# Kernel optimization log

Hardware: AMD Instinct MI355X
Metric: run time of the kernel (lower is better)

The kernel has to match this reference:

```python
import jax, jax.numpy as jnp
import numpy as np

EPS_H = 1.0   # smooth Heaviside / delta regularization
MAX_ITER = 10


def _chan_vese_step(phi, I, dt, lam):
    # phi, I: [B, 512, H, W]
    px = jnp.gradient(phi, axis=3)
    py = jnp.gradient(phi, axis=2)
    nrm = jnp.sqrt(px * px + py * py + 1e-8)
    curv = jnp.gradient(px / nrm, axis=3) + jnp.gradient(py / nrm, axis=2)
    # smooth Heaviside and region means (per batch, per channel)
    H = 0.5 * (1.0 + (2.0 / jnp.pi) * jnp.arctan(phi / EPS_H))
    a1 = jnp.sum(H, axis=(2, 3), keepdims=True)
    a2 = jnp.sum(1.0 - H, axis=(2, 3), keepdims=True)
    c1 = jnp.sum(I * H, axis=(2, 3), keepdims=True) / (a1 + 1e-8)
    c2 = jnp.sum(I * (1.0 - H), axis=(2, 3), keepdims=True) / (a2 + 1e-8)
    delta = (EPS_H / jnp.pi) / (phi * phi + EPS_H * EPS_H)
    force = curv - lam * (I - c1) ** 2 + lam * (I - c2) ** 2
    return phi + dt * delta * force


def setup_inputs() -> dict:
    key = jax.random.key(0)
    ks = jax.random.split(key, 6)
    B, C, Hh, Ww = 8, 256, 64, 64
    contour = jax.random.normal(ks[0], (B, C, Hh, Ww), dtype=jnp.float32)
    g = jax.random.normal(ks[1], (B, C, Hh, Ww), dtype=jnp.float32)
    x = jax.random.normal(ks[2], (B, 2 * C, Hh, Ww), dtype=jnp.float32)
    dt = jnp.array([0.1], dtype=jnp.float32)
    lambda_ = jnp.array([1.0], dtype=jnp.float32)
    # 1x1 conv weights (no bias), stored as [out_ch, in_ch]
    g_w = jax.random.normal(ks[3], (512, C), dtype=jnp.float32) / np.sqrt(C)
    x_w = jax.random.normal(ks[4], (512, 2 * C), dtype=jnp.float32) / np.sqrt(2 * C)
    c_w = jax.random.normal(ks[5], (512, C), dtype=jnp.float32) / np.sqrt(C)
    return {"contour": contour, "g": g, "x": x, "dt": dt, "lambda_": lambda_,
            "g_w": g_w, "x_w": x_w, "c_w": c_w}


def reference(contour, g, x, dt, lambda_, g_w, x_w, c_w):
    # z = relu(g_conv(g)) + x_conv(x); 1x1 convs are per-pixel GEMMs
    z = jax.nn.relu(jnp.einsum('bchw,oc->bohw', g, g_w)) \
        + jnp.einsum('bchw,oc->bohw', x, x_w)
    phi0 = jnp.einsum('bchw,oc->bohw', contour, c_w)
    # bicubic resize of phi0 to z's spatial size is identity (same H, W)
    dts = dt[0]
    lam = lambda_[0]
    def step(phi, _):
        return _chan_vese_step(phi, z, dts, lam), None
    phi, _ = jax.lax.scan(step, phi0, None, length=MAX_ITER)
    return jax.nn.sigmoid(phi)
```

## Files before the change

kernel.cpp:

```cpp
#include <hip/hip_runtime.h>
#include <math.h>

#define PIX 4096
#define O_CH 512
#define CV_PITCH 80
#define CV_SSTR 20
#define NY_PITCH 36

#define WOFF_G 0
#define WOFF_X 131072
#define WOFF_C 393216
#define W_ELEMS 524288

typedef __attribute__((ext_vector_type(8))) short s16x8;
typedef __attribute__((ext_vector_type(4))) float f32x4;
typedef __attribute__((ext_vector_type(2))) float f32x2;

__device__ __forceinline__ unsigned cvt_pk_bf16(float a, float b) {
  unsigned r;
  asm("v_cvt_pk_bf16_f32 %0, %1, %2" : "=v"(r) : "v"(a), "v"(b));
  return r;
}

__global__ __launch_bounds__(256) void conv_w(
    const float* __restrict__ gw, const float* __restrict__ xw,
    const float* __restrict__ cw,
    ushort* __restrict__ WH, ushort* __restrict__ WL)
{
  const int r = blockIdx.y;
  const float* src = (r == 0) ? gw : ((r == 1) ? xw : cw);
  const int n4 = (r == 1) ? 65536 : 32768;
  const int doff = (r == 0) ? WOFF_G : ((r == 1) ? WOFF_X : WOFF_C);
  const int i = blockIdx.x * 256 + threadIdx.x;
  if (i >= n4) return;
  float4 v = ((const float4*)src)[i];
  unsigned h01 = cvt_pk_bf16(v.x, v.y);
  unsigned h23 = cvt_pk_bf16(v.z, v.w);
  float l0 = v.x - __uint_as_float(h01 << 16);
  float l1 = v.y - __uint_as_float(h01 & 0xffff0000u);
  float l2 = v.z - __uint_as_float(h23 << 16);
  float l3 = v.w - __uint_as_float(h23 & 0xffff0000u);
  unsigned lo01 = cvt_pk_bf16(l0, l1);
  unsigned lo23 = cvt_pk_bf16(l2, l3);
  ((uint2*)(WH + doff))[i] = make_uint2(h01, h23);
  ((uint2*)(WL + doff))[i] = make_uint2(lo01, lo23);
}

__global__ __launch_bounds__(256, 2) void mfma_gemm_all(
    const float* __restrict__ g, const float* __restrict__ x,
    const float* __restrict__ contour,
    const ushort* __restrict__ WHg, const ushort* __restrict__ WLg,
    float* __restrict__ z, float* __restrict__ phi0)
{
  __shared__ ushort WHs[8192], WLs[8192], AHs[8192], ALs[8192];
  const int t = threadIdx.x;
  const int lane = t & 63, wave = t >> 6;
  const int wm = wave >> 1, wn = wave & 1;
  const int rowA = lane & 15, kg = lane >> 4;
  const int pb = blockIdx.x * 128, ob = blockIdx.y * 128;
  const int bz = blockIdx.z;
  const bool isZ = bz < 8;
  const int b = isZ ? bz : bz - 8;

  const int woff1 = isZ ? WOFF_G : WOFF_C;
  const int K1 = 256;
  const float* A1 = (isZ ? g : contour) + (size_t)b * K1 * PIX;
  const int K2 = 512;
  const float* A2 = isZ ? x + (size_t)b * K2 * PIX : nullptr;
  float* out = (isZ ? z : phi0) + (size_t)b * O_CH * PIX;

  f32x4 acc[4][4];
#pragma unroll
  for (int mi = 0; mi < 4; ++mi)
#pragma unroll
    for (int ni = 0; ni < 4; ++ni) acc[mi][ni] = (f32x4){0.f, 0.f, 0.f, 0.f};

  for (int pass = 0; pass < 2; ++pass) {
    if (pass == 1 && A2 == nullptr) break;
    const int K = pass ? K2 : K1;
    const int woff = pass ? WOFF_X : woff1;
    const float* A = pass ? A2 : A1;

    for (int kb = 0; kb < K; kb += 64) {
      {
        const int o_r = t >> 1, hf = t & 1;
        const size_t wbase = (size_t)woff + (size_t)(ob + o_r) * K + kb + hf * 32;
        const ushort* whrow = WHg + wbase;
        const ushort* wlrow = WLg + wbase;
#pragma unroll
        for (int i = 0; i < 4; ++i) {
          int idx = o_r * 64 + (((hf * 4 + i) ^ (o_r & 7)) << 3);
          *(s16x8*)&WHs[idx] = *(const s16x8*)(whrow + i * 8);
          *(s16x8*)&WLs[idx] = *(const s16x8*)(wlrow + i * 8);
        }
      }
#pragma unroll
      for (int ph = 0; ph < 2; ++ph) {
        const int rp = ph * 64 + lane;
        const float* ac = A + (size_t)kb * PIX + pb + rp;
#pragma unroll
        for (int ch = 0; ch < 2; ++ch) {
          const int kloc0 = ch * 32 + wave * 8;
          float v[8];
#pragma unroll
          for (int j = 0; j < 8; ++j) v[j] = ac[(size_t)(kloc0 + j) * PIX];
          unsigned h[4], l[4];
#pragma unroll
          for (int j2 = 0; j2 < 4; ++j2) {
            h[j2] = cvt_pk_bf16(v[2 * j2], v[2 * j2 + 1]);
            float lo0 = v[2 * j2] - __uint_as_float(h[j2] << 16);
            float lo1 = v[2 * j2 + 1] - __uint_as_float(h[j2] & 0xffff0000u);
            l[j2] = cvt_pk_bf16(lo0, lo1);
          }
          int grp = ch * 4 + wave;
          int idx = rp * 64 + ((grp ^ (rp & 7)) << 3);
          *(uint4*)&AHs[idx] = make_uint4(h[0], h[1], h[2], h[3]);
          *(uint4*)&ALs[idx] = make_uint4(l[0], l[1], l[2], l[3]);
        }
      }
      __syncthreads();
#pragma unroll
      for (int ks = 0; ks < 2; ++ks) {
        s16x8 wh[4], wlv[4], ah[4], alv[4];
#pragma unroll
        for (int mi = 0; mi < 4; ++mi) {
          int row = wm * 64 + mi * 16 + rowA;
          int idx = row * 64 + (((ks * 4 + kg) ^ (row & 7)) << 3);
          wh[mi]  = *(const s16x8*)&WHs[idx];
          wlv[mi] = *(const s16x8*)&WLs[idx];
        }
#pragma unroll
        for (int ni = 0; ni < 4; ++ni) {
          int row = wn * 64 + ni * 16 + rowA;
          int idx = row * 64 + (((ks * 4 + kg) ^ (row & 7)) << 3);
          ah[ni]  = *(const s16x8*)&AHs[idx];
          alv[ni] = *(const s16x8*)&ALs[idx];
        }
#pragma unroll
        for (int mi = 0; mi < 4; ++mi)
#pragma unroll
          for (int ni = 0; ni < 4; ++ni) {
            acc[mi][ni] = __builtin_amdgcn_mfma_f32_16x16x32_bf16(wh[mi],  ah[ni],  acc[mi][ni], 0, 0, 0);
            acc[mi][ni] = __builtin_amdgcn_mfma_f32_16x16x32_bf16(wh[mi],  alv[ni], acc[mi][ni], 0, 0, 0);
            acc[mi][ni] = __builtin_amdgcn_mfma_f32_16x16x32_bf16(wlv[mi], ah[ni],  acc[mi][ni], 0, 0, 0);
          }
      }
      __syncthreads();
    }
    if (pass == 0 && isZ) {
#pragma unroll
      for (int mi = 0; mi < 4; ++mi)
#pragma unroll
        for (int ni = 0; ni < 4; ++ni)
#pragma unroll
          for (int r = 0; r < 4; ++r) acc[mi][ni][r] = fmaxf(acc[mi][ni][r], 0.f);
    }
  }
  const int orow = (lane >> 4) * 4, pcol = lane & 15;
#pragma unroll
  for (int mi = 0; mi < 4; ++mi)
#pragma unroll
    for (int ni = 0; ni < 4; ++ni)
#pragma unroll
      for (int r = 0; r < 4; ++r)
        out[(size_t)(ob + wm * 64 + mi * 16 + orow + r) * PIX +
            pb + wn * 64 + ni * 16 + pcol] = acc[mi][ni][r];
}

__device__ __forceinline__ float fast_atan(float x) {
  float a = __builtin_fabsf(x);
  float inv = __builtin_amdgcn_rcpf(a);
  bool big = a > 1.f;
  float tt = big ? inv : a;
  float t2 = tt * tt;
  float p = fmaf(t2, 0.0208351f, -0.0851330f);
  p = fmaf(t2, p, 0.1801410f);
  p = fmaf(t2, p, -0.3302995f);
  p = fmaf(t2, p, 0.9998660f);
  p = p * tt;
  float r = big ? (1.57079632679f - p) : p;
  return __builtin_copysignf(r, x);
}

__global__ __launch_bounds__(256, 4) void chanvese(
    const float* __restrict__ zb, float* __restrict__ ob,
    const float* __restrict__ dtp, const float* __restrict__ lamp)
{
  __shared__ float phi_l[64 * CV_PITCH];
  __shared__ unsigned ny_l[64 * NY_PITCH];
  __shared__ float red[12];
  const int t = threadIdx.x;
  const int lane = t & 63, wv = t >> 6;
  const int row = t >> 2, s = t & 3;
  const size_t gbase = (size_t)blockIdx.x * PIX + row * 64 + s * 16;
  const float dtv = dtp[0], lam = lamp[0];
  const float INV_PI = 0.31830988618379067f;
  const float dtpi = dtv * INV_PI;
  const float fy = (row == 0 || row == 63) ? 1.f : 0.5f;
  const float exl = (s == 0) ? 2.f : 1.f;
  const float exr = (s == 3) ? 2.f : 1.f;
  const int my  = row * CV_PITCH + s * CV_SSTR;
  const int ub  = ((row == 0) ? 0 : row - 1) * CV_PITCH + s * CV_SSTR;
  const int db  = ((row == 63) ? 63 : row + 1) * CV_PITCH + s * CV_SSTR;
  const int myn = row * NY_PITCH + s * 8;
  const int ubn = ((row == 0) ? 0 : row - 1) * NY_PITCH + s * 8;
  const int dbn = ((row == 63) ? 63 : row + 1) * NY_PITCH + s * 8;
  const f32x2 eps2 = {1e-8f, 1e-8f};

  f32x2 I2[8], ph2[8], nx2[8];
#pragma unroll
  for (int q = 0; q < 4; ++q) {
    f32x4 iv = *(const f32x4*)(zb + gbase + q * 4);
    f32x4 pv = *(const f32x4*)(ob + gbase + q * 4);
    I2[2 * q]     = (f32x2){iv[0], iv[1]};
    I2[2 * q + 1] = (f32x2){iv[2], iv[3]};
    ph2[2 * q]     = (f32x2){pv[0], pv[1]};
    ph2[2 * q + 1] = (f32x2){pv[2], pv[3]};
    *(f32x4*)&phi_l[my + q * 4] = pv;
  }
  float sI = 0.f, s_at = 0.f, s_iat = 0.f;
#pragma unroll
  for (int p = 0; p < 8; ++p) {
    sI += I2[p].x + I2[p].y;
    float a0 = fast_atan(ph2[p].x), a1 = fast_atan(ph2[p].y);
    s_at += a0 + a1;
    s_iat = fmaf(I2[p].x, a0, fmaf(I2[p].y, a1, s_iat));
  }
#pragma unroll
  for (int off = 32; off; off >>= 1) {
    sI += __shfl_xor(sI, off);
    s_at += __shfl_xor(s_at, off);
    s_iat += __shfl_xor(s_iat, off);
  }
  if (lane == 0) { red[wv] = s_at; red[4 + wv] = s_iat; red[8 + wv] = sI; }
  __syncthreads();
  float S_at = red[0] + red[1] + red[2] + red[3];
  float S_iat = red[4] + red[5] + red[6] + red[7];
  const float sumI = red[8] + red[9] + red[10] + red[11];

  for (int it = 0; it < 10; ++it) {
    float a1 = fmaf(INV_PI, S_at, 2048.f);
    float sIH = fmaf(INV_PI, S_iat, 0.5f * sumI);
    float c1 = sIH * __builtin_amdgcn_rcpf(a1 + 1e-8f);
    float c2 = (sumI - sIH) * __builtin_amdgcn_rcpf(4096.f - a1 + 1e-8f);
    float lam12 = lam * (c1 - c2);
    float ms12 = -(c1 + c2);

    float ls = __shfl(ph2[7].y, lane - 1);
    float rs = __shfl(ph2[0].x, lane + 1);
    float lb = (s == 0) ? ph2[0].x : ls;
    float rb = (s == 3) ? ph2[7].y : rs;
    unsigned nyp[8];
#pragma unroll
    for (int q = 0; q < 4; ++q) {
      f32x4 uv = *(const f32x4*)&phi_l[ub + q * 4];
      f32x4 dv = *(const f32x4*)&phi_l[db + q * 4];
#pragma unroll
      for (int e = 0; e < 2; ++e) {
        const int p = 2 * q + e;
        f32x2 u2 = (f32x2){uv[2 * e], uv[2 * e + 1]};
        f32x2 d2 = (f32x2){dv[2 * e], dv[2 * e + 1]};
        f32x2 py = (d2 - u2) * fy;
        f32x2 L = {(p == 0) ? lb : ph2[p - 1].y, ph2[p].x};
        f32x2 R = {ph2[p].y, (p == 7) ? rb : ph2[p + 1].x};
        f32x2 px = (R - L) * 0.5f;
        if (p == 0) px.x *= exl;
        if (p == 7) px.y *= exr;
        f32x2 qq = px * px + (py * py + eps2);
        f32x2 rn = {__builtin_amdgcn_rsqf(qq.x), __builtin_amdgcn_rsqf(qq.y)};
        nx2[p] = px * rn;
        f32x2 nyv = py * rn;
        nyp[p] = cvt_pk_bf16(nyv.x, nyv.y);
      }
    }
    *(uint4*)&ny_l[myn]     = make_uint4(nyp[0], nyp[1], nyp[2], nyp[3]);
    *(uint4*)&ny_l[myn + 4] = make_uint4(nyp[4], nyp[5], nyp[6], nyp[7]);
    __syncthreads();

    float nls = __shfl(nx2[7].y, lane - 1);
    float nrs = __shfl(nx2[0].x, lane + 1);
    float nlb = (s == 0) ? nx2[0].x : nls;
    float nrb = (s == 3) ? nx2[7].y : nrs;
    f32x2 inc_at2 = {0.f, 0.f}, inc_iat2 = {0.f, 0.f};
#pragma unroll
    for (int h = 0; h < 2; ++h) {
      uint4 au = *(const uint4*)&ny_l[ubn + 4 * h];
      uint4 ad = *(const uint4*)&ny_l[dbn + 4 * h];
      unsigned ua[4] = {au.x, au.y, au.z, au.w};
      unsigned ud[4] = {ad.x, ad.y, ad.z, ad.w};
      f32x2 phs[4];
#pragma unroll
      for (int e = 0; e < 4; ++e) {
        const int p = 4 * h + e;
        f32x2 nyu = {__uint_as_float(ua[e] << 16), __uint_as_float(ua[e] & 0xffff0000u)};
        f32x2 nyd = {__uint_as_float(ud[e] << 16), __uint_as_float(ud[e] & 0xffff0000u)};
        f32x2 dny = (nyd - nyu) * fy;
        f32x2 L = {(p == 0) ? nlb : nx2[p - 1].y, nx2[p].x};
        f32x2 R = {nx2[p].y, (p == 7) ? nrb : nx2[p + 1].x};
        f32x2 dnx = (R - L) * 0.5f;
        if (p == 0) dnx.x *= exl;
        if (p == 7) dnx.y *= exr;
        f32x2 curv = dnx + dny;
        f32x2 c = ph2[p];
        f32x2 den = c * c + (f32x2){1.f, 1.f};
        f32x2 rcd = {__builtin_amdgcn_rcpf(den.x), __builtin_amdgcn_rcpf(den.y)};
        f32x2 tI = I2[p] * 2.f + ms12;
        f32x2 force = tI * lam12 + curv;
        f32x2 dphi = (rcd * dtpi) * force;
        f32x2 pn = c + dphi;
        ph2[p] = pn;
        phs[e] = pn;
        f32x2 da = dphi * rcd;
        inc_at2 += da;
        inc_iat2 = I2[p] * da + inc_iat2;
      }
      if (it < 9) {
        *(f32x4*)&phi_l[my + 8 * h] =
            (f32x4){phs[0].x, phs[0].y, phs[1].x, phs[1].y};
        *(f32x4*)&phi_l[my + 8 * h + 4] =
            (f32x4){phs[2].x, phs[2].y, phs[3].x, phs[3].y};
      }
    }
    if (it < 9) {
      float inc_at = inc_at2.x + inc_at2.y;
      float inc_iat = inc_iat2.x + inc_iat2.y;
#pragma unroll
      for (int off = 32; off; off >>= 1) {
        inc_at += __shfl_xor(inc_at, off);
        inc_iat += __shfl_xor(inc_iat, off);
      }
      if (lane == 0) { red[2 * wv] = inc_at; red[2 * wv + 1] = inc_iat; }
      __syncthreads();
      S_at += red[0] + red[2] + red[4] + red[6];
      S_iat += red[1] + red[3] + red[5] + red[7];
    }
  }

#pragma unroll
  for (int q = 0; q < 4; ++q) {
    f32x2 pa = ph2[2 * q], pb2 = ph2[2 * q + 1];
    float o0 = 1.f / (1.f + exp2f(pa.x * -1.44269504089f));
    float o1 = 1.f / (1.f + exp2f(pa.y * -1.44269504089f));
    float o2 = 1.f / (1.f + exp2f(pb2.x * -1.44269504089f));
    float o3 = 1.f / (1.f + exp2f(pb2.y * -1.44269504089f));
    *(float4*)(ob + gbase + q * 4) = make_float4(o0, o1, o2, o3);
  }
}

extern "C" void kernel_launch(void* const* d_in, const int* in_sizes, int n_in,
                              void* d_out, int out_size, void* d_ws, size_t ws_size,
                              hipStream_t stream)
{
  const float* contour = (const float*)d_in[0];
  const float* g       = (const float*)d_in[1];
  const float* x       = (const float*)d_in[2];
  const float* dt      = (const float*)d_in[3];
  const float* lam     = (const float*)d_in[4];
  const float* g_w     = (const float*)d_in[5];
  const float* x_w     = (const float*)d_in[6];
  const float* c_w     = (const float*)d_in[7];
  float* out = (float*)d_out;
  float* z   = (float*)d_ws;
  ushort* WH = (ushort*)(z + (size_t)8 * O_CH * PIX);
  ushort* WL = WH + W_ELEMS;

  conv_w<<<dim3(256, 3), dim3(256), 0, stream>>>(g_w, x_w, c_w, WH, WL);
  mfma_gemm_all<<<dim3(32, 4, 16), dim3(256), 0, stream>>>(
      g, x, contour, WH, WL, z, out);
  chanvese<<<dim3(4096), dim3(256), 0, stream>>>(z, out, dt, lam);
}
```

Before: 246.0 us.

## Software-pipeline activation loads in GEMM with register prefetch of next K-step

Flattens the two-pass K loop into one step loop of 12 or 4 steps and prefetches the next step's fp32 activation tile into registers while the MFMAs run on the current shared-memory tile. The goal is to hide global load latency behind the matrix math. It raises register pressure under launch_bounds(256,2), which may cause spills or lower occupancy. It also makes a minor explicit vector broadcast change in the Chan-Vese step.

```diff
diff --git a/kernel.cpp b/kernel.cpp
--- a/kernel.cpp
+++ b/kernel.cpp
@@ -63,11 +63,10 @@
   const int b = isZ ? bz : bz - 8;
 
   const int woff1 = isZ ? WOFF_G : WOFF_C;
-  const int K1 = 256;
-  const float* A1 = (isZ ? g : contour) + (size_t)b * K1 * PIX;
-  const int K2 = 512;
-  const float* A2 = isZ ? x + (size_t)b * K2 * PIX : nullptr;
+  const float* A1 = (isZ ? g : contour) + (size_t)b * 256 * PIX;
+  const float* A2 = x + (size_t)(isZ ? b : 0) * 512 * PIX;
   float* out = (isZ ? z : phi0) + (size_t)b * O_CH * PIX;
+  const int nsteps = isZ ? 12 : 4;
 
   f32x4 acc[4][4];
 #pragma unroll
@@ -75,79 +74,104 @@
 #pragma unroll
     for (int ni = 0; ni < 4; ++ni) acc[mi][ni] = (f32x4){0.f, 0.f, 0.f, 0.f};
 
-  for (int pass = 0; pass < 2; ++pass) {
-    if (pass == 1 && A2 == nullptr) break;
-    const int K = pass ? K2 : K1;
-    const int woff = pass ? WOFF_X : woff1;
-    const float* A = pass ? A2 : A1;
-
-    for (int kb = 0; kb < K; kb += 64) {
-      {
-        const int o_r = t >> 1, hf = t & 1;
-        const size_t wbase = (size_t)woff + (size_t)(ob + o_r) * K + kb + hf * 32;
-        const ushort* whrow = WHg + wbase;
-        const ushort* wlrow = WLg + wbase;
-#pragma unroll
-        for (int i = 0; i < 4; ++i) {
-          int idx = o_r * 64 + (((hf * 4 + i) ^ (o_r & 7)) << 3);
-          *(s16x8*)&WHs[idx] = *(const s16x8*)(whrow + i * 8);
-          *(s16x8*)&WLs[idx] = *(const s16x8*)(wlrow + i * 8);
+  float pf[2][2][8];
+
+#pragma unroll
+  for (int ph = 0; ph < 2; ++ph) {
+    const float* acp = A1 + pb + ph * 64 + lane;
+#pragma unroll
+    for (int ch = 0; ch < 2; ++ch) {
+      const int kl0 = ch * 32 + wave * 8;
+#pragma unroll
+      for (int j = 0; j < 8; ++j)
+        pf[ph][ch][j] = acp[(size_t)(kl0 + j) * PIX];
+    }
+  }
+
+  for (int st = 0; st < nsteps; ++st) {
+    const bool s2 = st >= 4;
+    const int K = s2 ? 512 : 256;
+    const int woff = s2 ? WOFF_X : woff1;
+    const int kb = (s2 ? st - 4 : st) * 64;
+
+    {
+      const int o_r = t >> 1, hf = t & 1;
+      const size_t wbase = (size_t)woff + (size_t)(ob + o_r) * K + kb + hf * 32;
+      const ushort* whrow = WHg + wbase;
+      const ushort* wlrow = WLg + wbase;
+#pragma unroll
+      for (int i = 0; i < 4; ++i) {
+        int idx = o_r * 64 + (((hf * 4 + i) ^ (o_r & 7)) << 3);
+        *(s16x8*)&WHs[idx] = *(const s16x8*)(whrow + i * 8);
+        *(s16x8*)&WLs[idx] = *(const s16x8*)(wlrow + i * 8);
+      }
+    }
+#pragma unroll
+    for (int ph = 0; ph < 2; ++ph) {
+      const int rp = ph * 64 + lane;
+#pragma unroll
+      for (int ch = 0; ch < 2; ++ch) {
+        unsigned h[4], l[4];
+#pragma unroll
+        for (int j2 = 0; j2 < 4; ++j2) {
+          float v0 = pf[ph][ch][2 * j2], v1 = pf[ph][ch][2 * j2 + 1];
+          h[j2] = cvt_pk_bf16(v0, v1);
+          float lo0 = v0 - __uint_as_float(h[j2] << 16);
+          float lo1 = v1 - __uint_as_float(h[j2] & 0xffff0000u);
+          l[j2] = cvt_pk_bf16(lo0, lo1);
         }
-      }
+        int grp = ch * 4 + wave;
+        int idx = rp * 64 + ((grp ^ (rp & 7)) << 3);
+        *(uint4*)&AHs[idx] = make_uint4(h[0], h[1], h[2], h[3]);
+        *(uint4*)&ALs[idx] = make_uint4(l[0], l[1], l[2], l[3]);
+      }
+    }
+    __syncthreads();
+
+    if (st + 1 < nsteps) {
+      const bool n2 = (st + 1) >= 4;
+      const float* Ab = n2 ? A2 : A1;
+      const int kbn = (n2 ? st + 1 - 4 : st + 1) * 64;
 #pragma unroll
       for (int ph = 0; ph < 2; ++ph) {
-        const int rp = ph * 64 + lane;
-        const float* ac = A + (size_t)kb * PIX + pb + rp;
+        const float* acp = Ab + (size_t)kbn * PIX + pb + ph * 64 + lane;
 #pragma unroll
         for (int ch = 0; ch < 2; ++ch) {
-          const int kloc0 = ch * 32 + wave * 8;
-          float v[8];
-#pragma unroll
-          for (int j = 0; j < 8; ++j) v[j] = ac[(size_t)(kloc0 + j) * PIX];
-          unsigned h[4], l[4];
-#pragma unroll
-          for (int j2 = 0; j2 < 4; ++j2) {
-            h[j2] = cvt_pk_bf16(v[2 * j2], v[2 * j2 + 1]);
-            float lo0 = v[2 * j2] - __uint_as_float(h[j2] << 16);
-            float lo1 = v[2 * j2 + 1] - __uint_as_float(h[j2] & 0xffff0000u);
-            l[j2] = cvt_pk_bf16(lo0, lo1);
-          }
-          int grp = ch * 4 + wave;
-          int idx = rp * 64 + ((grp ^ (rp & 7)) << 3);
-          *(uint4*)&AHs[idx] = make_uint4(h[0], h[1], h[2], h[3]);
-          *(uint4*)&ALs[idx] = make_uint4(l[0], l[1], l[2], l[3]);
+          const int kl0 = ch * 32 + wave * 8;
+#pragma unroll
+          for (int j = 0; j < 8; ++j)
+            pf[ph][ch][j] = acp[(size_t)(kl0 + j) * PIX];
         }
       }
-      __syncthreads();
-#pragma unroll
-      for (int ks = 0; ks < 2; ++ks) {
-        s16x8 wh[4], wlv[4], ah[4], alv[4];
-#pragma unroll
-        for (int mi = 0; mi < 4; ++mi) {
-          int row = wm * 64 + mi * 16 + rowA;
-          int idx = row * 64 + (((ks * 4 + kg) ^ (row & 7)) << 3);
-          wh[mi]  = *(const s16x8*)&WHs[idx];
-          wlv[mi] = *(const s16x8*)&WLs[idx];
+    }
+
+#pragma unroll
+    for (int ks = 0; ks < 2; ++ks) {
+      s16x8 wh[4], wlv[4], ah[4], alv[4];
+#pragma unroll
+      for (int mi = 0; mi < 4; ++mi) {
+        int row = wm * 64 + mi * 16 + rowA;
+        int idx = row * 64 + (((ks * 4 + kg) ^ (row & 7)) << 3);
+        wh[mi]  = *(const s16x8*)&WHs[idx];
+        wlv[mi] = *(const s16x8*)&WLs[idx];
+      }
+#pragma unroll
+      for (int ni = 0; ni < 4; ++ni) {
+        int row = wn * 64 + ni * 16 + rowA;
+        int idx = row * 64 + (((ks * 4 + kg) ^ (row & 7)) << 3);
+        ah[ni]  = *(const s16x8*)&AHs[idx];
+        alv[ni] = *(const s16x8*)&ALs[idx];
+      }
+#pragma unroll
+      for (int mi = 0; mi < 4; ++mi)
+#pragma unroll
+        for (int ni = 0; ni < 4; ++ni) {
+          acc[mi][ni] = __builtin_amdgcn_mfma_f32_16x16x32_bf16(wh[mi],  ah[ni],  acc[mi][ni], 0, 0, 0);
+          acc[mi][ni] = __builtin_amdgcn_mfma_f32_16x16x32_bf16(wh[mi],  alv[ni], acc[mi][ni], 0, 0, 0);
+          acc[mi][ni] = __builtin_amdgcn_mfma_f32_16x16x32_bf16(wlv[mi], ah[ni],  acc[mi][ni], 0, 0, 0);
         }
-#pragma unroll
-        for (int ni = 0; ni < 4; ++ni) {
-          int row = wn * 64 + ni * 16 + rowA;
-          int idx = row * 64 + (((ks * 4 + kg) ^ (row & 7)) << 3);
-          ah[ni]  = *(const s16x8*)&AHs[idx];
-          alv[ni] = *(const s16x8*)&ALs[idx];
-        }
-#pragma unroll
-        for (int mi = 0; mi < 4; ++mi)
-#pragma unroll
-          for (int ni = 0; ni < 4; ++ni) {
-            acc[mi][ni] = __builtin_amdgcn_mfma_f32_16x16x32_bf16(wh[mi],  ah[ni],  acc[mi][ni], 0, 0, 0);
-            acc[mi][ni] = __builtin_amdgcn_mfma_f32_16x16x32_bf16(wh[mi],  alv[ni], acc[mi][ni], 0, 0, 0);
-            acc[mi][ni] = __builtin_amdgcn_mfma_f32_16x16x32_bf16(wlv[mi], ah[ni],  acc[mi][ni], 0, 0, 0);
-          }
-      }
-      __syncthreads();
-    }
-    if (pass == 0 && isZ) {
+    }
+    if (isZ && st == 3) {
 #pragma unroll
       for (int mi = 0; mi < 4; ++mi)
 #pragma unroll
@@ -155,7 +179,9 @@
 #pragma unroll
           for (int r = 0; r < 4; ++r) acc[mi][ni][r] = fmaxf(acc[mi][ni][r], 0.f);
     }
-  }
+    __syncthreads();
+  }
+
   const int orow = (lane >> 4) * 4, pcol = lane & 15;
 #pragma unroll
   for (int mi = 0; mi < 4; ++mi)
@@ -304,7 +330,7 @@
         f32x2 c = ph2[p];
         f32x2 den = c * c + (f32x2){1.f, 1.f};
         f32x2 rcd = {__builtin_amdgcn_rcpf(den.x), __builtin_amdgcn_rcpf(den.y)};
-        f32x2 tI = I2[p] * 2.f + ms12;
+        f32x2 tI = I2[p] * 2.f + (f32x2){ms12, ms12};
         f32x2 force = tI * lam12 + curv;
         f32x2 dphi = (rcd * dtpi) * force;
         f32x2 pn = c + dphi;
```

Result: no change. 247.9 us (+0.8%).
